# Kernel tuning notes

Measured on AMD Instinct MI355X. Metric: run time of the kernel, lower is better.

## Reference

```python
import jax, jax.numpy as jnp
import numpy as np

NUM_HEADS = 16
CLAMP = 1e4


def setup_inputs() -> dict:
    key = jax.random.key(0)
    ks = jax.random.split(key, 8)
    B, Nq, Nkv, Cq, Ckv = 4, 2048, 2048, 1024, 768
    s_q = 1.0 / np.sqrt(Cq)
    s_kv = 1.0 / np.sqrt(Ckv)
    return {
        "query": jax.random.normal(ks[0], (B, Nq, Cq), jnp.float32),
        "key_value": jax.random.normal(ks[1], (B, Nkv, Ckv), jnp.float32),
        "Wq": jax.random.normal(ks[2], (Cq, Cq), jnp.float32) * s_q,
        "bq": jnp.zeros((Cq,), jnp.float32),
        "Wk": jax.random.normal(ks[3], (Ckv, Cq), jnp.float32) * s_kv,
        "bk": jnp.zeros((Cq,), jnp.float32),
        "Wv": jax.random.normal(ks[4], (Ckv, Cq), jnp.float32) * s_kv,
        "bv": jnp.zeros((Cq,), jnp.float32),
        "Wo": jax.random.normal(ks[5], (Cq, Cq), jnp.float32) * s_q,
        "bo": jnp.zeros((Cq,), jnp.float32),
    }


def reference(query, key_value, Wq, bq, Wk, bk, Wv, bv, Wo, bo):
    B, Nq, Cq = query.shape
    Nkv = key_value.shape[1]
    H = NUM_HEADS
    D = Cq // H
    scale = D ** (-0.5)

    # projections -> [B, H, N, D]
    q = (query @ Wq + bq).reshape(B, Nq, H, D).transpose(0, 2, 1, 3)
    k = (key_value @ Wk + bk).reshape(B, Nkv, H, D).transpose(0, 2, 1, 3)
    v = (key_value @ Wv + bv).reshape(B, Nkv, H, D).transpose(0, 2, 1, 3)

    # scores [B, H, Nq, Nkv] with clamp (mask=None path)
    attn = jnp.einsum("bhqd,bhkd->bhqk", q, k) * scale
    attn = jnp.clip(attn, -CLAMP, CLAMP)
    attn = jax.nn.softmax(attn, axis=-1)
    # NaN fallback: replace with uniform attention if any NaN present
    attn = jnp.where(jnp.any(jnp.isnan(attn)),
                     jnp.asarray(1.0 / Nkv, attn.dtype), attn)

    # weighted sum -> [B, Nq, Cq]
    x = jnp.einsum("bhqk,bhkd->bqhd", attn, v).reshape(B, Nq, Cq)
    return x @ Wo + bo
```

## Files before the change

### kernel.cpp

```cpp
#include <hip/hip_runtime.h>
#include <hip/hip_bf16.h>
#include <stdint.h>


typedef unsigned short u16;
typedef __attribute__((ext_vector_type(2))) float f32x2;
typedef __attribute__((ext_vector_type(4))) short bf16x4;
typedef __attribute__((ext_vector_type(8))) short bf16x8;
typedef __attribute__((ext_vector_type(4))) float f32x4;
typedef __attribute__((ext_vector_type(16))) float f32x16;

__device__ __forceinline__ u16 f2bf(float x) {
  union { float f; uint32_t u; } c; c.f = x;
  uint32_t r = c.u + 0x7fffu + ((c.u >> 16) & 1u);
  return (u16)(r >> 16);
}

__device__ __forceinline__ uint32_t pkbf(float a, float b) {
#if __has_builtin(__builtin_amdgcn_cvt_pk_bf16_f32)
  typedef __attribute__((ext_vector_type(2))) __bf16 bf2;
  bf2 r = __builtin_amdgcn_cvt_pk_bf16_f32(a, b);
  return __builtin_bit_cast(uint32_t, r);
#else
  return (uint32_t)f2bf(a) | ((uint32_t)f2bf(b) << 16);
#endif
}

__device__ __forceinline__ void gld16(const void* g, void* l) {
  __builtin_amdgcn_global_load_lds(
      (const __attribute__((address_space(1))) void*)g,
      (__attribute__((address_space(3))) void*)l, 16, 0, 0);
}

__device__ __forceinline__ void cvt_body(const float* __restrict__ in,
                                         u16* __restrict__ out, int blk) {
  int i = (blk * 256 + threadIdx.x) * 8;
  float4 a = *(const float4*)(in + i);
  float4 b = *(const float4*)(in + i + 4);
  union { u16 u[8]; uint4 v; } o;
  o.u[0] = f2bf(a.x); o.u[1] = f2bf(a.y); o.u[2] = f2bf(a.z); o.u[3] = f2bf(a.w);
  o.u[4] = f2bf(b.x); o.u[5] = f2bf(b.y); o.u[6] = f2bf(b.z); o.u[7] = f2bf(b.w);
  *(uint4*)(out + i) = o.v;
}

__device__ __forceinline__ void transpose_body(const float* __restrict__ in,
                                               u16* __restrict__ out,
                                               int R, int C, int bx, int by) {
  __shared__ float tile[64][65];
  int c0 = bx * 64, r0 = by * 64;
  #pragma unroll
  for (int it = 0; it < 16; it++) {
    int idx = threadIdx.x + it * 256;
    int lr = idx >> 6, lc = idx & 63;
    tile[lr][lc] = in[(size_t)(r0 + lr) * C + c0 + lc];
  }
  __syncthreads();
  #pragma unroll
  for (int it = 0; it < 16; it++) {
    int idx = threadIdx.x + it * 256;
    int lc = idx >> 6, lr = idx & 63;
    out[(size_t)(c0 + lc) * R + r0 + lr] = f2bf(tile[lr][lc]);
  }
}

__global__ void prep_kernel(const float* __restrict__ query,
                            const float* __restrict__ key_value,
                            const float* __restrict__ Wq, const float* __restrict__ Wk,
                            const float* __restrict__ Wv, const float* __restrict__ Wo,
                            u16* qb, u16* kvb, u16* WqT, u16* WkT, u16* WvT, u16* WoT) {
  int blk = blockIdx.x;
  if (blk < 4096) { cvt_body(query, qb, blk); return; }
  if (blk < 7168) { cvt_body(key_value, kvb, blk - 4096); return; }
  if (blk < 7424) { int lo = blk - 7168; transpose_body(Wq, WqT, 1024, 1024, lo & 15, lo >> 4); return; }
  if (blk < 7616) { int lo = blk - 7424; transpose_body(Wk, WkT, 768, 1024, lo & 15, lo >> 4); return; }
  if (blk < 7808) { int lo = blk - 7616; transpose_body(Wv, WvT, 768, 1024, lo & 15, lo >> 4); return; }
  { int lo = blk - 7808; transpose_body(Wo, WoT, 1024, 1024, lo & 15, lo >> 4); return; }
}

template<bool SWAP>
__device__ __forceinline__ void gemm_kloop(const u16* __restrict__ A,
                                           const u16* __restrict__ BT,
                                           int K, char* smem, f32x4 (&acc)[4][4],
                                           int m0, int n0, int tid) {
  const u16* ap[4]; const u16* bp[4]; int ldA[4], ldB[4];
  #pragma unroll
  for (int it2 = 0; it2 < 4; it2++) {
    int s = it2 * 256 + tid;
    int row = s >> 3, cl = (s & 7) ^ (row & 7);
    ap[it2] = A + (size_t)(m0 + row) * K + cl * 8;
    bp[it2] = BT + (size_t)(n0 + row) * K + cl * 8;
    ldA[it2] = s * 16;
    ldB[it2] = 16384 + s * 16;
  }
  const int w = tid >> 6, l = tid & 63;
  const int lm = l & 15, lq = l >> 4;
  const int wr = w >> 1, wc = w & 1;
  int abase[4], bbase[4];
  #pragma unroll
  for (int i = 0; i < 4; i++) {
    int m = wr * 64 + i * 16 + lm;
    abase[i] = m * 128 + ((lq ^ (m & 7)) << 4);
    int n = wc * 64 + i * 16 + lm;
    bbase[i] = 16384 + n * 128 + ((lq ^ (n & 7)) << 4);
  }
  for (int k0 = 0; k0 < K; k0 += 64) {
    #pragma unroll
    for (int it2 = 0; it2 < 4; it2++) {
      gld16(ap[it2], smem + ldA[it2]);
      gld16(bp[it2], smem + ldB[it2]);
      ap[it2] += 64; bp[it2] += 64;
    }
    __syncthreads();
    #pragma unroll
    for (int kk = 0; kk < 2; kk++) {
      bf16x8 af[4], bf[4];
      #pragma unroll
      for (int i = 0; i < 4; i++)
        af[i] = *(const bf16x8*)(smem + (abase[i] ^ (kk << 6)));
      #pragma unroll
      for (int j = 0; j < 4; j++)
        bf[j] = *(const bf16x8*)(smem + (bbase[j] ^ (kk << 6)));
      #pragma unroll
      for (int i = 0; i < 4; i++)
        #pragma unroll
        for (int j = 0; j < 4; j++) {
          if (SWAP)
            acc[i][j] = __builtin_amdgcn_mfma_f32_16x16x32_bf16(bf[j], af[i], acc[i][j], 0, 0, 0);
          else
            acc[i][j] = __builtin_amdgcn_mfma_f32_16x16x32_bf16(af[i], bf[j], acc[i][j], 0, 0, 0);
        }
    }
    __syncthreads();
  }
}

__global__ __launch_bounds__(256, 3)
void gemm_qkv(const u16* __restrict__ qb, const u16* __restrict__ kvb,
              const u16* __restrict__ WqT, const u16* __restrict__ WkT,
              const u16* __restrict__ WvT,
              const float* __restrict__ bq, const float* __restrict__ bk,
              const float* __restrict__ bv,
              u16* __restrict__ Qb, u16* __restrict__ Kbf, u16* __restrict__ Vt,
              float qscale) {
  extern __shared__ __align__(16) char smem[];
  const int tid = threadIdx.x;
  const int w = tid >> 6, l = tid & 63;
  const int lm = l & 15, lq = l >> 4;
  const int m0 = blockIdx.y * 128, n0 = blockIdx.x * 128;
  const int wr = w >> 1, wc = w & 1;
  const int z = blockIdx.z;
  f32x4 acc[4][4] = {};

  u16* etile = (u16*)(smem + w * 9216);
  const int xr = l >> 3, cc = (l & 7) ^ xr;

  if (z < 2) {
    const u16* A = (z == 0) ? qb : kvb;
    const u16* BT = (z == 0) ? WqT : WkT;
    const float* bias = (z == 0) ? bq : bk;
    u16* out = (z == 0) ? Qb : Kbf;
    const float scale = (z == 0) ? qscale : 1.0f;
    const int K = (z == 0) ? 1024 : 768;
    gemm_kloop<true>(A, BT, K, smem, acc, m0, n0, tid);
    #pragma unroll
    for (int j = 0; j < 4; j++) {
      float4 b4 = *(const float4*)&bias[n0 + wc * 64 + j * 16 + lq * 4];
      #pragma unroll
      for (int i = 0; i < 4; i++) {
        uint2 pkd;
        pkd.x = pkbf((acc[i][j][0] + b4.x) * scale, (acc[i][j][1] + b4.y) * scale);
        pkd.y = pkbf((acc[i][j][2] + b4.z) * scale, (acc[i][j][3] + b4.w) * scale);
        *(uint2*)&etile[(i * 16 + lm) * 72 + j * 16 + lq * 4] = pkd;
      }
    }
    u16* gbase = out + (size_t)(m0 + wr * 64) * 1024 + n0 + wc * 64;
    #pragma unroll
    for (int co = 0; co < 8; co++) {
      int ml = co * 8 + xr;
      uint4 d = *(const uint4*)&etile[ml * 72 + cc * 8];
      *(uint4*)&gbase[(size_t)ml * 1024 + cc * 8] = d;
    }
  } else {
    gemm_kloop<false>(kvb, WvT, 768, smem, acc, m0, n0, tid);
    #pragma unroll
    for (int j = 0; j < 4; j++) {
      float bi = bv[n0 + wc * 64 + j * 16 + lm];
      #pragma unroll
      for (int i = 0; i < 4; i++) {
        uint2 pkd;
        pkd.x = pkbf(acc[i][j][0] + bi, acc[i][j][1] + bi);
        pkd.y = pkbf(acc[i][j][2] + bi, acc[i][j][3] + bi);
        *(uint2*)&etile[(j * 16 + lm) * 72 + i * 16 + lq * 4] = pkd;
      }
    }
    const int bb = m0 >> 11, mloc = (m0 & 2047) + wr * 64;
    u16* gbase = Vt + ((size_t)bb * 1024 + n0 + wc * 64) * 2048 + mloc;
    const int kvA = (cc >> 1) * 16 + (cc & 1) * 4;
    #pragma unroll
    for (int co = 0; co < 8; co++) {
      int dl = co * 8 + xr;
      uint2 dA = *(const uint2*)&etile[dl * 72 + kvA];
      uint2 dB = *(const uint2*)&etile[dl * 72 + kvA + 8];
      uint4 d = {dA.x, dA.y, dB.x, dB.y};
      *(uint4*)&gbase[(size_t)dl * 2048 + cc * 8] = d;
    }
  }
}

__global__ __launch_bounds__(256, 3)
void gemm_o(const u16* __restrict__ A, const u16* __restrict__ BT,
            const float* __restrict__ bias, float* __restrict__ Cout) {
  __shared__ __align__(16) char smem[32768];
  const int tid = threadIdx.x;
  const int w = tid >> 6, l = tid & 63;
  const int lm = l & 15, lq = l >> 4;
  const int m0 = blockIdx.y * 128, n0 = blockIdx.x * 128;
  const int wr = w >> 1, wc = w & 1;
  f32x4 acc[4][4] = {};
  gemm_kloop<false>(A, BT, 1024, smem, acc, m0, n0, tid);
  #pragma unroll
  for (int j = 0; j < 4; j++) {
    int gn = n0 + wc * 64 + j * 16 + lm;
    float bi = bias[gn];
    #pragma unroll
    for (int i = 0; i < 4; i++) {
      int gm = m0 + wr * 64 + i * 16 + lq * 4;
      #pragma unroll
      for (int r = 0; r < 4; r++)
        Cout[(size_t)(gm + r) * 1024 + gn] = acc[i][j][r] + bi;
    }
  }
}

__global__ __launch_bounds__(256, 2)
void attn_kernel(const u16* __restrict__ Q, const u16* __restrict__ Kb,
                 const u16* __restrict__ Vt, u16* __restrict__ X) {
  __shared__ __align__(16) char smem[32768];
  const int tid = threadIdx.x, w = tid >> 6, l = tid & 63;
  const int l31 = l & 31, h5 = l >> 5;
  const int bh = blockIdx.x, b = bh >> 4, h = bh & 15;
  const int q0 = blockIdx.y * 256 + w * 64;
  const int rx = l31 & 7;

  const u16* Kg = Kb + (size_t)b * 2048 * 1024 + h * 64;
  const u16* Vg = Vt + (size_t)bh * 64 * 2048;

  const u16 *kp0, *kp1, *vp0, *vp1;
  {
    int s = tid, r = s >> 3, c = (s & 7) ^ (r & 7);
    kp0 = Kg + (size_t)r * 1024 + c * 8;
    vp0 = Vg + (size_t)r * 2048 + c * 8;
    s = 256 + tid; r = s >> 3; c = (s & 7) ^ (r & 7);
    kp1 = Kg + (size_t)r * 1024 + c * 8;
    vp1 = Vg + (size_t)r * 2048 + c * 8;
  }
  const int kd0 = tid * 16, kd1 = (256 + tid) * 16;

  bf16x8 qfA[4], qfB[4];
  {
    const u16* qp = Q + ((size_t)(b * 2048 + q0 + l31)) * 1024 + h * 64 + h5 * 8;
    #pragma unroll
    for (int t = 0; t < 4; t++) qfA[t] = *(const bf16x8*)(qp + t * 16);
    qp += (size_t)32 * 1024;
    #pragma unroll
    for (int t = 0; t < 4; t++) qfB[t] = *(const bf16x8*)(qp + t * 16);
  }

  const int kvb2 = (l31 << 7) | ((rx ^ h5) << 4);
  const int vb2 = 16384 | (l31 << 7) | ((rx ^ h5) << 4);

  f32x16 xaccA[2] = {}, xaccB[2] = {};
  f32x2 lsA = {0.f, 0.f}, lsB = {0.f, 0.f};
  const f32x16 KZ = {};

  gld16(kp0, smem + kd0); gld16(kp1, smem + kd1);
  gld16(vp0, smem + 16384 + kd0); gld16(vp1, smem + 16384 + kd1);
  kp0 += 65536; kp1 += 65536; vp0 += 64; vp1 += 64;
  __syncthreads();

#define ATTN_STEP(CUR, DOPREF)                                                  \
  {                                                                             \
    if (DOPREF) {                                                               \
      const int nb = ((CUR) ^ 1) << 13;                                         \
      gld16(kp0, smem + nb + kd0); gld16(kp1, smem + nb + kd1);                 \
      gld16(vp0, smem + 16384 + nb + kd0); gld16(vp1, smem + 16384 + nb + kd1); \
      kp0 += 65536; kp1 += 65536; vp0 += 64; vp1 += 64;                         \
    }                                                                           \
    _Pragma("unroll")                                                           \
    for (int sub = 0; sub < 2; sub++) {                                         \
      const int km = ((CUR) << 13) | (sub << 12);                               \
      bf16x8 kf[4];                                                             \
      _Pragma("unroll")                                                         \
      for (int t = 0; t < 4; t++)                                               \
        kf[t] = *(const bf16x8*)(smem + (kvb2 ^ (km | (t << 5))));              \
      f32x16 st = __builtin_amdgcn_mfma_f32_32x32x16_bf16(kf[0], qfA[0], KZ, 0, 0, 0); \
      _Pragma("unroll")                                                         \
      for (int t = 1; t < 4; t++)                                               \
        st = __builtin_amdgcn_mfma_f32_32x32x16_bf16(kf[t], qfA[t], st, 0, 0, 0); \
      uint32_t pkA[8], pkB[8];                                                  \
      _Pragma("unroll")                                                         \
      for (int u = 0; u < 4; u++) {                                             \
        float p0 = __builtin_amdgcn_exp2f(st[4 * u + 0]);                       \
        float p1 = __builtin_amdgcn_exp2f(st[4 * u + 1]);                       \
        float p2 = __builtin_amdgcn_exp2f(st[4 * u + 2]);                       \
        float p3 = __builtin_amdgcn_exp2f(st[4 * u + 3]);                       \
        lsA += (f32x2){p0 + p2, p1 + p3};                                       \
        pkA[2 * u] = pkbf(p0, p1); pkA[2 * u + 1] = pkbf(p2, p3);               \
      }                                                                         \
      st = __builtin_amdgcn_mfma_f32_32x32x16_bf16(kf[0], qfB[0], KZ, 0, 0, 0); \
      _Pragma("unroll")                                                         \
      for (int t = 1; t < 4; t++)                                               \
        st = __builtin_amdgcn_mfma_f32_32x32x16_bf16(kf[t], qfB[t], st, 0, 0, 0); \
      _Pragma("unroll")                                                         \
      for (int u = 0; u < 4; u++) {                                             \
        float p0 = __builtin_amdgcn_exp2f(st[4 * u + 0]);                       \
        float p1 = __builtin_amdgcn_exp2f(st[4 * u + 1]);                       \
        float p2 = __builtin_amdgcn_exp2f(st[4 * u + 2]);                       \
        float p3 = __builtin_amdgcn_exp2f(st[4 * u + 3]);                       \
        lsB += (f32x2){p0 + p2, p1 + p3};                                       \
        pkB[2 * u] = pkbf(p0, p1); pkB[2 * u + 1] = pkbf(p2, p3);               \
      }                                                                         \
      _Pragma("unroll")                                                         \
      for (int c2 = 0; c2 < 2; c2++) {                                          \
        union { uint32_t d[4]; bf16x8 v; } pfA, pfB;                            \
        _Pragma("unroll")                                                       \
        for (int dd = 0; dd < 4; dd++) {                                        \
          pfA.d[dd] = pkA[4 * c2 + dd]; pfB.d[dd] = pkB[4 * c2 + dd];           \
        }                                                                       \
        const int vx = ((sub << 2) | (c2 << 1)) << 4;                           \
        _Pragma("unroll")                                                       \
        for (int dt = 0; dt < 2; dt++) {                                        \
          bf16x8 vf = *(const bf16x8*)(smem +                                   \
              (vb2 ^ (((CUR) << 13) | (dt << 12) | vx)));                       \
          xaccA[dt] = __builtin_amdgcn_mfma_f32_32x32x16_bf16(vf, pfA.v, xaccA[dt], 0, 0, 0); \
          xaccB[dt] = __builtin_amdgcn_mfma_f32_32x32x16_bf16(vf, pfB.v, xaccB[dt], 0, 0, 0); \
        }                                                                       \
      }                                                                         \
    }                                                                           \
    __syncthreads();                                                            \
  }

  for (int itp = 0; itp < 15; itp++) {
    ATTN_STEP(0, true)
    ATTN_STEP(1, true)
  }
  ATTN_STEP(0, true)
  ATTN_STEP(1, false)
#undef ATTN_STEP

  {
    float lsum = lsA[0] + lsA[1];
    const float inv = 1.0f / (lsum + __shfl_xor(lsum, 32));
    u16* xp = X + ((size_t)(b * 2048 + q0 + l31)) * 1024 + h * 64;
    #pragma unroll
    for (int dt = 0; dt < 2; dt++)
      #pragma unroll
      for (int g = 0; g < 4; g++) {
        const int d0 = dt * 32 + g * 8 + h5 * 4;
        uint2 o;
        o.x = pkbf(xaccA[dt][4 * g + 0] * inv, xaccA[dt][4 * g + 1] * inv);
        o.y = pkbf(xaccA[dt][4 * g + 2] * inv, xaccA[dt][4 * g + 3] * inv);
        *(uint2*)(xp + d0) = o;
      }
  }
  {
    float lsum = lsB[0] + lsB[1];
    const float inv = 1.0f / (lsum + __shfl_xor(lsum, 32));
    u16* xp = X + ((size_t)(b * 2048 + q0 + 32 + l31)) * 1024 + h * 64;
    #pragma unroll
    for (int dt = 0; dt < 2; dt++)
      #pragma unroll
      for (int g = 0; g < 4; g++) {
        const int d0 = dt * 32 + g * 8 + h5 * 4;
        uint2 o;
        o.x = pkbf(xaccB[dt][4 * g + 0] * inv, xaccB[dt][4 * g + 1] * inv);
        o.y = pkbf(xaccB[dt][4 * g + 2] * inv, xaccB[dt][4 * g + 3] * inv);
        *(uint2*)(xp + d0) = o;
      }
  }
}

extern "C" void kernel_launch(void* const* d_in, const int* in_sizes, int n_in,
                              void* d_out, int out_size, void* d_ws, size_t ws_size,
                              hipStream_t stream) {
  const float* query     = (const float*)d_in[0];
  const float* key_value = (const float*)d_in[1];
  const float* Wq = (const float*)d_in[2];
  const float* bq = (const float*)d_in[3];
  const float* Wk = (const float*)d_in[4];
  const float* bk = (const float*)d_in[5];
  const float* Wv = (const float*)d_in[6];
  const float* bv = (const float*)d_in[7];
  const float* Wo = (const float*)d_in[8];
  const float* bo = (const float*)d_in[9];
  float* out = (float*)d_out;

  char* ws = (char*)d_ws;
  size_t off = 0;
  auto alloc = [&](size_t bytes) -> void* {
    void* p = ws + off; off += (bytes + 255) & ~(size_t)255; return p;
  };
  u16* qb  = (u16*)alloc((size_t)8192 * 1024 * 2);
  u16* kvb = (u16*)alloc((size_t)8192 * 768 * 2);
  u16* WqT = (u16*)alloc((size_t)1024 * 1024 * 2);
  u16* WkT = (u16*)alloc((size_t)1024 * 768 * 2);
  u16* WvT = (u16*)alloc((size_t)1024 * 768 * 2);
  u16* WoT = (u16*)alloc((size_t)1024 * 1024 * 2);
  u16* Qb  = (u16*)alloc((size_t)8192 * 1024 * 2);
  u16* Kbf = (u16*)alloc((size_t)8192 * 1024 * 2);
  u16* Vt  = (u16*)alloc((size_t)8192 * 1024 * 2);
  u16* Xb  = (u16*)alloc((size_t)8192 * 1024 * 2);

  prep_kernel<<<8064, 256, 0, stream>>>(query, key_value, Wq, Wk, Wv, Wo,
                                        qb, kvb, WqT, WkT, WvT, WoT);

  const float qscale = 0.125f * 1.4426950408889634f;
  gemm_qkv<<<dim3(8, 64, 3), 256, 36864, stream>>>(qb, kvb, WqT, WkT, WvT,
                                                   bq, bk, bv, Qb, Kbf, Vt, qscale);

  attn_kernel<<<dim3(64, 8), 256, 0, stream>>>(Qb, Kbf, Vt, Xb);

  gemm_o<<<dim3(8, 64), 256, 0, stream>>>(Xb, WoT, bo, out);
}
```

Baseline: 289.2 us.

## Halve attention query tile per wave, double grid, raise occupancy, add setprio

Each wave now processes 32 query rows instead of 64, so the attention grid doubles to 1024 blocks and launch bounds allow 4 blocks per CU. This cuts register pressure and raises the number of resident waves. The cost is that every K/V tile staged into LDS is reused by half as many query rows, which doubles K/V global traffic. s_setprio is also placed around the MFMA sections so waves in matrix phases get issue priority over waves doing exp work.

```diff
diff --git a/kernel.cpp b/kernel.cpp
--- a/kernel.cpp
+++ b/kernel.cpp
@@ -232,14 +232,14 @@
   }
 }
 
-__global__ __launch_bounds__(256, 2)
+__global__ __launch_bounds__(256, 4)
 void attn_kernel(const u16* __restrict__ Q, const u16* __restrict__ Kb,
                  const u16* __restrict__ Vt, u16* __restrict__ X) {
   __shared__ __align__(16) char smem[32768];
   const int tid = threadIdx.x, w = tid >> 6, l = tid & 63;
   const int l31 = l & 31, h5 = l >> 5;
   const int bh = blockIdx.x, b = bh >> 4, h = bh & 15;
-  const int q0 = blockIdx.y * 256 + w * 64;
+  const int q0 = blockIdx.y * 128 + w * 32;
   const int rx = l31 & 7;
 
   const u16* Kg = Kb + (size_t)b * 2048 * 1024 + h * 64;
@@ -256,21 +256,18 @@
   }
   const int kd0 = tid * 16, kd1 = (256 + tid) * 16;
 
-  bf16x8 qfA[4], qfB[4];
+  bf16x8 qfA[4];
   {
     const u16* qp = Q + ((size_t)(b * 2048 + q0 + l31)) * 1024 + h * 64 + h5 * 8;
     #pragma unroll
     for (int t = 0; t < 4; t++) qfA[t] = *(const bf16x8*)(qp + t * 16);
-    qp += (size_t)32 * 1024;
-    #pragma unroll
-    for (int t = 0; t < 4; t++) qfB[t] = *(const bf16x8*)(qp + t * 16);
   }
 
   const int kvb2 = (l31 << 7) | ((rx ^ h5) << 4);
   const int vb2 = 16384 | (l31 << 7) | ((rx ^ h5) << 4);
 
-  f32x16 xaccA[2] = {}, xaccB[2] = {};
-  f32x2 lsA = {0.f, 0.f}, lsB = {0.f, 0.f};
+  f32x16 xaccA[2] = {};
+  f32x2 lsA = {0.f, 0.f};
   const f32x16 KZ = {};
 
   gld16(kp0, smem + kd0); gld16(kp1, smem + kd1);
@@ -293,11 +290,13 @@
       _Pragma("unroll")                                                         \
       for (int t = 0; t < 4; t++)                                               \
         kf[t] = *(const bf16x8*)(smem + (kvb2 ^ (km | (t << 5))));              \
+      __builtin_amdgcn_s_setprio(1);                                            \
       f32x16 st = __builtin_amdgcn_mfma_f32_32x32x16_bf16(kf[0], qfA[0], KZ, 0, 0, 0); \
       _Pragma("unroll")                                                         \
       for (int t = 1; t < 4; t++)                                               \
         st = __builtin_amdgcn_mfma_f32_32x32x16_bf16(kf[t], qfA[t], st, 0, 0, 0); \
-      uint32_t pkA[8], pkB[8];                                                  \
+      __builtin_amdgcn_s_setprio(0);                                            \
+      uint32_t pkA[8];                                                          \
       _Pragma("unroll")                                                         \
       for (int u = 0; u < 4; u++) {                                             \
         float p0 = __builtin_amdgcn_exp2f(st[4 * u + 0]);                       \
@@ -307,34 +306,20 @@
         lsA += (f32x2){p0 + p2, p1 + p3};                                       \
         pkA[2 * u] = pkbf(p0, p1); pkA[2 * u + 1] = pkbf(p2, p3);               \
       }                                                                         \
-      st = __builtin_amdgcn_mfma_f32_32x32x16_bf16(kf[0], qfB[0], KZ, 0, 0, 0); \
-      _Pragma("unroll")                                                         \
-      for (int t = 1; t < 4; t++)                                               \
-        st = __builtin_amdgcn_mfma_f32_32x32x16_bf16(kf[t], qfB[t], st, 0, 0, 0); \
-      _Pragma("unroll")                                                         \
-      for (int u = 0; u < 4; u++) {                                             \
-        float p0 = __builtin_amdgcn_exp2f(st[4 * u + 0]);                       \
-        float p1 = __builtin_amdgcn_exp2f(st[4 * u + 1]);                       \
-        float p2 = __builtin_amdgcn_exp2f(st[4 * u + 2]);                       \
-        float p3 = __builtin_amdgcn_exp2f(st[4 * u + 3]);                       \
-        lsB += (f32x2){p0 + p2, p1 + p3};                                       \
-        pkB[2 * u] = pkbf(p0, p1); pkB[2 * u + 1] = pkbf(p2, p3);               \
-      }                                                                         \
       _Pragma("unroll")                                                         \
       for (int c2 = 0; c2 < 2; c2++) {                                          \
-        union { uint32_t d[4]; bf16x8 v; } pfA, pfB;                            \
+        union { uint32_t d[4]; bf16x8 v; } pfA;                                 \
         _Pragma("unroll")                                                       \
-        for (int dd = 0; dd < 4; dd++) {                                        \
-          pfA.d[dd] = pkA[4 * c2 + dd]; pfB.d[dd] = pkB[4 * c2 + dd];           \
-        }                                                                       \
+        for (int dd = 0; dd < 4; dd++) pfA.d[dd] = pkA[4 * c2 + dd];            \
         const int vx = ((sub << 2) | (c2 << 1)) << 4;                           \
+        __builtin_amdgcn_s_setprio(1);                                          \
         _Pragma("unroll")                                                       \
         for (int dt = 0; dt < 2; dt++) {                                        \
           bf16x8 vf = *(const bf16x8*)(smem +                                   \
               (vb2 ^ (((CUR) << 13) | (dt << 12) | vx)));                       \
           xaccA[dt] = __builtin_amdgcn_mfma_f32_32x32x16_bf16(vf, pfA.v, xaccA[dt], 0, 0, 0); \
-          xaccB[dt] = __builtin_amdgcn_mfma_f32_32x32x16_bf16(vf, pfB.v, xaccB[dt], 0, 0, 0); \
         }                                                                       \
+        __builtin_amdgcn_s_setprio(0);                                          \
       }                                                                         \
     }                                                                           \
     __syncthreads();                                                            \
@@ -360,21 +345,6 @@
         uint2 o;
         o.x = pkbf(xaccA[dt][4 * g + 0] * inv, xaccA[dt][4 * g + 1] * inv);
         o.y = pkbf(xaccA[dt][4 * g + 2] * inv, xaccA[dt][4 * g + 3] * inv);
-        *(uint2*)(xp + d0) = o;
-      }
-  }
-  {
-    float lsum = lsB[0] + lsB[1];
-    const float inv = 1.0f / (lsum + __shfl_xor(lsum, 32));
-    u16* xp = X + ((size_t)(b * 2048 + q0 + 32 + l31)) * 1024 + h * 64;
-    #pragma unroll
-    for (int dt = 0; dt < 2; dt++)
-      #pragma unroll
-      for (int g = 0; g < 4; g++) {
-        const int d0 = dt * 32 + g * 8 + h5 * 4;
-        uint2 o;
-        o.x = pkbf(xaccB[dt][4 * g + 0] * inv, xaccB[dt][4 * g + 1] * inv);
-        o.y = pkbf(xaccB[dt][4 * g + 2] * inv, xaccB[dt][4 * g + 3] * inv);
         *(uint2*)(xp + d0) = o;
       }
   }
@@ -418,7 +388,7 @@
   gemm_qkv<<<dim3(8, 64, 3), 256, 36864, stream>>>(qb, kvb, WqT, WkT, WvT,
                                                    bq, bk, bv, Qb, Kbf, Vt, qscale);
 
-  attn_kernel<<<dim3(64, 8), 256, 0, stream>>>(Qb, Kbf, Vt, Xb);
+  attn_kernel<<<dim3(64, 16), 256, 0, stream>>>(Qb, Kbf, Vt, Xb);
 
   gemm_o<<<dim3(8, 64), 256, 0, stream>>>(Xb, WoT, bo, out);
 }
```

After: 295.0 us. 2.0% more time.
